# Kernel tuning notes

Measured on AMD Instinct MI355X. Metric: run time of the kernel, lower is better.

The kernel has to match this reference:

```python
import jax, jax.numpy as jnp
import numpy as np

DIM = 2048
N_HEADS = 16
QK_NOPE = 128
QK_ROPE = 64
V_DIM = 128
QK_DIM = QK_NOPE + QK_ROPE  # 192
B, S = 2, 2048


def setup_inputs() -> dict:
    key = jax.random.key(0)
    ks = jax.random.split(key, 6)
    x = jax.random.normal(ks[0], (B, S, DIM), dtype=jnp.float32)
    # rotary angles: theta[j] = 10000^{-2j/d}, angle[p, j] = p * theta[j]
    inv_freq = 1.0 / (10000.0 ** (np.arange(0, QK_ROPE, 2, dtype=np.float32) / QK_ROPE))
    freqs = jnp.asarray(np.arange(S, dtype=np.float32)[:, None] * inv_freq[None, :])  # [S, QK_ROPE//2]
    # additive causal mask
    mask = jnp.where(jnp.tril(jnp.ones((S, S), dtype=bool)), 0.0, -1e9).astype(jnp.float32)
    sc = 1.0 / np.sqrt(DIM)
    wq = jax.random.normal(ks[1], (DIM, N_HEADS * QK_DIM), dtype=jnp.float32) * sc
    wk = jax.random.normal(ks[2], (DIM, N_HEADS * QK_DIM), dtype=jnp.float32) * sc
    wv = jax.random.normal(ks[3], (DIM, N_HEADS * V_DIM), dtype=jnp.float32) * sc
    wo = jax.random.normal(ks[4], (N_HEADS * V_DIM, DIM), dtype=jnp.float32) * (1.0 / np.sqrt(N_HEADS * V_DIM))
    return {"x": x, "start_pos": 0, "freqs": freqs, "mask": mask,
            "wq": wq, "wk": wk, "wv": wv, "wo": wo}


def _apply_rope(t, freqs):
    # t: [B, S, H, D_rope]; freqs: [S, D_rope//2] angles
    b, s, h, d = t.shape
    tr = t.reshape(b, s, h, d // 2, 2)
    cos = jnp.cos(freqs)[None, :, None, :]
    sin = jnp.sin(freqs)[None, :, None, :]
    out = jnp.stack([tr[..., 0] * cos - tr[..., 1] * sin,
                     tr[..., 0] * sin + tr[..., 1] * cos], axis=-1)
    return out.reshape(b, s, h, d)


def reference(x, start_pos, freqs, mask, wq, wk, wv, wo):
    b, s, _ = x.shape
    xq = x @ wq  # [B,S,H*QK_DIM]
    xk = x @ wk
    xv = (x @ wv).reshape(b, s, N_HEADS, V_DIM)
    qnope, qrope = jnp.split(xq, [N_HEADS * QK_NOPE], axis=-1)
    knope, krope = jnp.split(xk, [N_HEADS * QK_NOPE], axis=-1)
    qnope = qnope.reshape(b, s, N_HEADS, QK_NOPE)
    knope = knope.reshape(b, s, N_HEADS, QK_NOPE)
    qrope = _apply_rope(qrope.reshape(b, s, N_HEADS, QK_ROPE), freqs)
    krope = _apply_rope(krope.reshape(b, s, N_HEADS, QK_ROPE), freqs)
    q = jnp.concatenate([qnope, qrope], axis=-1)  # [B,S,H,QK_DIM]
    k = jnp.concatenate([knope, krope], axis=-1)
    scale = 1.0 / jnp.sqrt(jnp.asarray(QK_DIM, dtype=q.dtype))
    scores = jnp.einsum('bqhd,bkhd->bhqk', q, k) * scale
    scores = scores + mask[None, None, :, :]
    attn = jax.nn.softmax(scores.astype(jnp.float32), axis=-1).astype(scores.dtype)
    out = jnp.einsum('bhqk,bkhd->bqhd', attn, xv)  # [B,S,H,V_DIM]
    out = out.reshape(b, s, N_HEADS * V_DIM)
    return out @ wo
```

## Files before the change

### kernel.cpp

```cpp
#include <hip/hip_runtime.h>
#include <hip/hip_bf16.h>

typedef __attribute__((ext_vector_type(4))) float f32x4;
typedef __attribute__((ext_vector_type(8))) short s16x8;
typedef unsigned int u32;
typedef unsigned short u16;

#define GLDS16(gp, lp) __builtin_amdgcn_global_load_lds(                         \
    (const __attribute__((address_space(1))) u32*)(gp),                          \
    (__attribute__((address_space(3))) u32*)(lp), 16, 0, 0)
#define VMCNT4 asm volatile("s_waitcnt vmcnt(4)" ::: "memory")
#define VMCNT0 asm volatile("s_waitcnt vmcnt(0)" ::: "memory")
#define LGKM8  asm volatile("s_waitcnt lgkmcnt(8)" ::: "memory")
#define LGKM0  asm volatile("s_waitcnt lgkmcnt(0)" ::: "memory")
#define SBAR   __builtin_amdgcn_sched_barrier(0)

__device__ __forceinline__ u16 f2bf(float f) {
    u32 u = __builtin_bit_cast(u32, f);
    u32 r = (u + 0x7FFFu + ((u >> 16) & 1u)) >> 16;
    return (u16)r;
}
__device__ __forceinline__ float bf2f(u16 h) {
    u32 u = ((u32)h) << 16;
    return __builtin_bit_cast(float, u);
}

__global__ __launch_bounds__(256) void prep(const float4* __restrict__ x,
                                            ushort4* __restrict__ xb4,
                                            const float* __restrict__ wq,
                                            const float* __restrict__ wk,
                                            const float* __restrict__ wv,
                                            const float* __restrict__ wo,
                                            u16* __restrict__ WT,
                                            u16* __restrict__ woT) {
    __shared__ float tile[32][33];
    int bid = blockIdx.x;
    if (bid < 8192) {
        int i = bid * 256 + threadIdx.x;
        float4 v = x[i];
        ushort4 o;
        o.x = f2bf(v.x); o.y = f2bf(v.y); o.z = f2bf(v.z); o.w = f2bf(v.w);
        xb4[i] = o;
        return;
    }
    bid -= 8192;
    const float* src;
    u16* dst;
    int N, bx, by;
    if (bid < 6144)       { src = wq; dst = WT;                        N = 3072; bx = bid % 96; by = bid / 96; }
    else if (bid < 12288) { bid -= 6144;  src = wk; dst = WT + (size_t)3072 * 2048; N = 3072; bx = bid % 96; by = bid / 96; }
    else if (bid < 16384) { bid -= 12288; src = wv; dst = WT + (size_t)6144 * 2048; N = 2048; bx = bid % 64; by = bid / 64; }
    else                  { bid -= 16384; src = wo; dst = woT;         N = 2048; bx = bid % 64; by = bid / 64; }
    int n0 = bx * 32, k0 = by * 32;
    int tx = threadIdx.x & 31, ty = threadIdx.x >> 5;
#pragma unroll
    for (int i = 0; i < 4; ++i)
        tile[ty + i * 8][tx] = src[(size_t)(k0 + ty + i * 8) * N + n0 + tx];
    __syncthreads();
#pragma unroll
    for (int i = 0; i < 4; ++i) {
        int n = ty + i * 8;
        dst[(size_t)(n0 + n) * 2048 + k0 + tx] = f2bf(tile[tx][n]);
    }
}

__global__ __launch_bounds__(512, 2) void gemm_qkv(const u16* __restrict__ A,
                                                   const u16* __restrict__ W,
                                                   u16* __restrict__ Qh,
                                                   u16* __restrict__ Kh,
                                                   u16* __restrict__ Vn) {
    __shared__ __align__(16) u16 S[2][2][2][128 * 64];
    const int tid = threadIdx.x, lane = tid & 63, wid = tid >> 6;
    const int l15 = lane & 15, l4 = lane >> 4;
    const int id = blockIdx.x;
    const int nt = ((id & 7) << 2) + ((id >> 3) & 3);
    const int mt = id >> 5;
    const int bm0 = mt << 8, bn0 = nt << 8;
    const int wr = wid >> 2, wc = wid & 3;
    f32x4 acc[8][4] = {};

    auto stageH = [&](int mat, int tt, int h) {
        const int kc = tt << 6, p = tt & 1;
        const u16* G = mat ? W : A;
        const int rbase = (mat ? bn0 : bm0) + (h << 7);
        u16* Ld = S[mat][p][h];
#pragma unroll
        for (int j = 0; j < 2; ++j) {
            int c = j * 512 + tid;
            int row = c >> 3, ch = c & 7;
            int cs = ch ^ (row & 7);
            GLDS16(G + (size_t)(rbase + row) * 2048 + kc + cs * 8,
                   (char*)Ld + (j * 512 + wid * 64) * 16);
        }
    };

    s16x8 af[2][2], bfr[4][2];

#define RDA(P, I)                                                              \
    _Pragma("unroll") for (int mm = 0; mm < 2; ++mm)                           \
    _Pragma("unroll") for (int kk = 0; kk < 2; ++kk) {                         \
        int r7 = ((I) * 2 + mm) * 16 + l15;                                    \
        int byt = r7 * 128 + (((kk * 4 + l4) ^ (r7 & 7)) << 4);                \
        af[mm][kk] = *(const s16x8*)((const char*)S[0][P][wr] + byt);          \
    }
#define RDB(P)                                                                 \
    _Pragma("unroll") for (int n = 0; n < 4; ++n)                              \
    _Pragma("unroll") for (int kk = 0; kk < 2; ++kk) {                         \
        int r7 = (wc & 1) * 64 + n * 16 + l15;                                 \
        int byt = r7 * 128 + (((kk * 4 + l4) ^ (r7 & 7)) << 4);                \
        bfr[n][kk] = *(const s16x8*)((const char*)S[1][P][wc >> 1] + byt);     \
    }
#define MF(I)                                                                  \
    __builtin_amdgcn_s_setprio(1);                                             \
    _Pragma("unroll") for (int mm = 0; mm < 2; ++mm)                           \
    _Pragma("unroll") for (int n = 0; n < 4; ++n)                              \
    _Pragma("unroll") for (int kk = 0; kk < 2; ++kk)                           \
        acc[(I) * 2 + mm][n] = __builtin_amdgcn_mfma_f32_16x16x32_bf16(        \
            af[mm][kk], bfr[n][kk], acc[(I) * 2 + mm][n], 0, 0, 0);            \
    __builtin_amdgcn_s_setprio(0);

    stageH(0, 0, 0); stageH(0, 0, 1); stageH(1, 0, 0); stageH(1, 0, 1);
    stageH(0, 1, 0); stageH(0, 1, 1);
    VMCNT4;
    __builtin_amdgcn_s_barrier();
    SBAR;

    for (int t = 0; t < 32; ++t) {
        const int p = t & 1;
        RDB(p); RDA(p, 0);
        if (t == 0) stageH(1, 1, 0);
        else if (t < 31) stageH(0, t + 1, 0);
        LGKM8; SBAR;
        __builtin_amdgcn_s_barrier();
        LGKM0; SBAR;
        MF(0); SBAR;
        __builtin_amdgcn_s_barrier();
        RDA(p, 1);
        if (t == 0) stageH(1, 1, 1);
        else if (t < 31) stageH(0, t + 1, 1);
        __builtin_amdgcn_s_barrier();
        LGKM0; SBAR;
        MF(1); SBAR;
        __builtin_amdgcn_s_barrier();
        RDA(p, 2);
        if (t < 30) stageH(1, t + 2, 0);
        __builtin_amdgcn_s_barrier();
        LGKM0; SBAR;
        MF(2); SBAR;
        __builtin_amdgcn_s_barrier();
        RDA(p, 3);
        if (t < 30) stageH(1, t + 2, 1);
        __builtin_amdgcn_s_barrier();
        LGKM0; SBAR;
        MF(3); SBAR;
        if (t < 31) {
            if (t < 30) { VMCNT4; } else { VMCNT0; }
            SBAR;
        }
        __builtin_amdgcn_s_barrier();
    }
#undef RDA
#undef RDB
#undef MF

#pragma unroll
    for (int m = 0; m < 8; ++m)
#pragma unroll
        for (int n = 0; n < 4; ++n)
#pragma unroll
            for (int r = 0; r < 4; ++r) {
                int row = bm0 + wr * 128 + m * 16 + l4 * 4 + r;
                int c = bn0 + wc * 64 + n * 16 + l15;
                float v = acc[m][n][r];
                if (bn0 >= 6144) {
                    Vn[(size_t)row * 2048 + (c - 6144)] = f2bf(v);
                } else {
                    u16* dst = (bn0 >= 3072) ? Kh : Qh;
                    int cc = (bn0 >= 3072) ? c - 3072 : c;
                    int b = row >> 11, s = row & 2047;
                    int h, d;
                    if (cc < 2048) { h = cc >> 7; d = cc & 127; }
                    else { int mm = cc - 2048; h = mm >> 6; d = 128 + (mm & 63); }
                    dst[(((size_t)b * 16 + h) * 2048 + s) * 192 + d] = f2bf(v);
                }
            }
}

__global__ __launch_bounds__(256) void gemm_bt_f32(const u16* __restrict__ A,
                                                   const u16* __restrict__ Bt,
                                                   float* __restrict__ C,
                                                   int M, int N, int K) {
    __shared__ __align__(16) u16 As[128 * 64];
    __shared__ __align__(16) u16 Bs[128 * 64];
    const int tid = threadIdx.x, lane = tid & 63, wid = tid >> 6;
    const int l15 = lane & 15, l4 = lane >> 4;
    const int bm0 = blockIdx.y << 7, bn0 = blockIdx.x << 7;
    const int wr = wid >> 1, wc = wid & 1;
    f32x4 acc[4][4] = {};
    const int nk = K >> 6;
    for (int t = 0; t < nk; ++t) {
        const int k0 = t << 6;
#pragma unroll
        for (int i = 0; i < 4; ++i) {
            int c = i * 256 + tid;
            int row = c >> 3, c8 = c & 7;
            GLDS16(A + (size_t)(bm0 + row) * K + k0 + c8 * 8,
                   (char*)As + (i * 256 + wid * 64) * 16);
        }
#pragma unroll
        for (int i = 0; i < 4; ++i) {
            int c = i * 256 + tid;
            int row = c >> 3, c8 = c & 7;
            GLDS16(Bt + (size_t)(bn0 + row) * K + k0 + c8 * 8,
                   (char*)Bs + (i * 256 + wid * 64) * 16);
        }
        __syncthreads();
#pragma unroll
        for (int kk = 0; kk < 64; kk += 32) {
            s16x8 af[4], bfr[4];
#pragma unroll
            for (int m = 0; m < 4; ++m)
                af[m] = *(const s16x8*)(As + (wr * 64 + m * 16 + l15) * 64 + kk + l4 * 8);
#pragma unroll
            for (int n = 0; n < 4; ++n)
                bfr[n] = *(const s16x8*)(Bs + (wc * 64 + n * 16 + l15) * 64 + kk + l4 * 8);
#pragma unroll
            for (int m = 0; m < 4; ++m)
#pragma unroll
                for (int n = 0; n < 4; ++n)
                    acc[m][n] = __builtin_amdgcn_mfma_f32_16x16x32_bf16(af[m], bfr[n],
                                                                        acc[m][n], 0, 0, 0);
        }
        __syncthreads();
    }
#pragma unroll
    for (int m = 0; m < 4; ++m)
#pragma unroll
        for (int n = 0; n < 4; ++n)
#pragma unroll
            for (int r = 0; r < 4; ++r) {
                int row = bm0 + wr * 64 + m * 16 + l4 * 4 + r;
                int col = bn0 + wc * 64 + n * 16 + l15;
                C[(size_t)row * N + col] = acc[m][n][r];
            }
}

__global__ __launch_bounds__(256) void rope_inplace(u16* __restrict__ T,
                                                    const float* __restrict__ freqs) {
    int idx = blockIdx.x * 256 + threadIdx.x;
    int j = idx & 31, s = (idx >> 5) & 2047, bh = idx >> 16;
    float ang = freqs[s * 32 + j];
    float c = cosf(ang), sn = sinf(ang);
    u32* p = (u32*)(T + ((size_t)bh * 2048 + s) * 192 + 128) + j;
    u32 v = *p;
    float t0 = bf2f((u16)(v & 0xffff)), t1 = bf2f((u16)(v >> 16));
    float o0 = t0 * c - t1 * sn;
    float o1 = t0 * sn + t1 * c;
    *p = (u32)f2bf(o0) | ((u32)f2bf(o1) << 16);
}

__global__ __launch_bounds__(256) void vtrans(const u16* __restrict__ Vn,
                                              u16* __restrict__ Vt) {
    __shared__ u16 tile[32][33];
    int s0 = blockIdx.x * 32, d0 = blockIdx.y * 32, bh = blockIdx.z;
    int b = bh >> 4, h = bh & 15;
    int tx = threadIdx.x & 31, ty = threadIdx.x >> 5;
#pragma unroll
    for (int i = 0; i < 4; ++i) {
        int s = ty + i * 8;
        tile[s][tx] = Vn[((size_t)b * 2048 + s0 + s) * 2048 + h * 128 + d0 + tx];
    }
    __syncthreads();
#pragma unroll
    for (int i = 0; i < 4; ++i) {
        int d = ty + i * 8;
        Vt[((size_t)bh * 128 + d0 + d) * 2048 + s0 + tx] = tile[tx][d];
    }
}

__global__ __launch_bounds__(256) void attn_fwd3(const u16* __restrict__ Qh,
                                                 const u16* __restrict__ Kh,
                                                 const u16* __restrict__ Vt,
                                                 u16* __restrict__ AO) {
    __shared__ __align__(16) u16 Ks[64 * 192];
    __shared__ __align__(16) u16 Vs[128 * 64];
    __shared__ __align__(16) u16 Ps[4][32 * 64];
    const int tid = threadIdx.x, lane = tid & 63, wid = tid >> 6;
    const int l15 = lane & 15, l4 = lane >> 4;
    const int id = blockIdx.x;
    const int bh = id & 31;
    const int qt = 15 - (id >> 5);
    const int q0 = qt << 7;
    const u16* Qb = Qh + ((size_t)bh * 2048 + q0 + wid * 32) * 192;
    const u16* Kb = Kh + (size_t)bh * 2048 * 192;
    const u16* Vb = Vt + (size_t)bh * 128 * 2048;

    s16x8 aq[2][6];
#pragma unroll
    for (int qg = 0; qg < 2; ++qg)
#pragma unroll
        for (int dk = 0; dk < 6; ++dk)
            aq[qg][dk] = *(const s16x8*)(Qb + (size_t)(qg * 16 + l15) * 192 + dk * 32 + l4 * 8);

    f32x4 acc[2][8] = {};
    float mrow[2][4], lpart[2][4];
#pragma unroll
    for (int qg = 0; qg < 2; ++qg)
#pragma unroll
        for (int r = 0; r < 4; ++r) { mrow[qg][r] = -1e30f; lpart[qg][r] = 0.f; }
    const float scale = 0.07216878364870322f;

    const int ntile = (qt + 1) << 1;
    for (int t = 0; t < ntile; ++t) {
        const int k0 = t << 6;
#pragma unroll
        for (int i = 0; i < 6; ++i) {
            int c = i * 256 + tid;
            int row = (u32)c / 24u, cc = c - row * 24;
            int cs = (cc & 24) | ((cc ^ row) & 7);
            GLDS16(Kb + (size_t)(k0 + row) * 192 + cs * 8,
                   (char*)Ks + (i * 256 + wid * 64) * 16);
        }
#pragma unroll
        for (int i = 0; i < 4; ++i) {
            int c = i * 256 + tid;
            int d = c >> 3, cc = c & 7;
            int cs = cc ^ (d & 7);
            GLDS16(Vb + (size_t)d * 2048 + k0 + cs * 8,
                   (char*)Vs + (i * 256 + wid * 64) * 16);
        }
        __syncthreads();

        if (q0 + wid * 32 + 31 >= k0) {
            f32x4 sc[2][4];
#pragma unroll
            for (int qg = 0; qg < 2; ++qg)
#pragma unroll
                for (int kg = 0; kg < 4; ++kg) sc[qg][kg] = f32x4{0.f, 0.f, 0.f, 0.f};
            __builtin_amdgcn_s_setprio(1);
#pragma unroll
            for (int dk = 0; dk < 6; ++dk) {
                s16x8 bk[4];
#pragma unroll
                for (int kg = 0; kg < 4; ++kg) {
                    int row = kg * 16 + l15;
                    int byt = (row * 384 + dk * 64 + l4 * 16) ^ ((row & 7) << 4);
                    bk[kg] = *(const s16x8*)((const char*)Ks + byt);
                }
#pragma unroll
                for (int qg = 0; qg < 2; ++qg)
#pragma unroll
                    for (int kg = 0; kg < 4; ++kg)
                        sc[qg][kg] = __builtin_amdgcn_mfma_f32_16x16x32_bf16(
                            aq[qg][dk], bk[kg], sc[qg][kg], 0, 0, 0);
            }
            __builtin_amdgcn_s_setprio(0);

            u16* Pw = Ps[wid];
#pragma unroll
            for (int qg = 0; qg < 2; ++qg) {
                const int qrow = q0 + wid * 32 + qg * 16 + l4 * 4;
                const bool domask = (k0 + 63 > qrow);
                float p[4][4], tm[4];
#pragma unroll
                for (int r = 0; r < 4; ++r) tm[r] = -1e30f;
#pragma unroll
                for (int kg = 0; kg < 4; ++kg)
#pragma unroll
                    for (int r = 0; r < 4; ++r) {
                        float v = sc[qg][kg][r] * scale;
                        if (domask && (k0 + kg * 16 + l15 > qrow + r)) v = -1e30f;
                        p[kg][r] = v;
                        tm[r] = fmaxf(tm[r], v);
                    }
#pragma unroll
                for (int off = 1; off < 16; off <<= 1)
#pragma unroll
                    for (int r = 0; r < 4; ++r)
                        tm[r] = fmaxf(tm[r], __shfl_xor(tm[r], off, 64));
                float mn[4];
                bool resc = false;
#pragma unroll
                for (int r = 0; r < 4; ++r) {
                    mn[r] = (tm[r] <= mrow[qg][r] + 8.f) ? mrow[qg][r] : tm[r];
                    resc |= (mn[r] > mrow[qg][r]);
                }
                if (__any(resc)) {
#pragma unroll
                    for (int r = 0; r < 4; ++r) {
                        float scl = __expf(mrow[qg][r] - mn[r]);
                        mrow[qg][r] = mn[r];
                        lpart[qg][r] *= scl;
#pragma unroll
                        for (int db = 0; db < 8; ++db) acc[qg][db][r] *= scl;
                    }
                }
#pragma unroll
                for (int kg = 0; kg < 4; ++kg)
#pragma unroll
                    for (int r = 0; r < 4; ++r) {
                        p[kg][r] = __expf(p[kg][r] - mrow[qg][r]);
                        lpart[qg][r] += p[kg][r];
                    }
#pragma unroll
                for (int kg = 0; kg < 4; ++kg)
#pragma unroll
                    for (int r = 0; r < 4; ++r) {
                        int row = qg * 16 + l4 * 4 + r;
                        int byt = ((row * 64 + kg * 16 + l15) * 2) ^ ((row & 7) << 4);
                        *(u16*)((char*)Pw + byt) = f2bf(p[kg][r]);
                    }
            }

            __builtin_amdgcn_s_setprio(1);
#pragma unroll
            for (int kk = 0; kk < 2; ++kk) {
                s16x8 ap[2];
#pragma unroll
                for (int qg = 0; qg < 2; ++qg) {
                    int row = qg * 16 + l15;
                    int byt = ((row * 64 + kk * 32 + l4 * 8) * 2) ^ ((row & 7) << 4);
                    ap[qg] = *(const s16x8*)((const char*)Pw + byt);
                }
#pragma unroll
                for (int db = 0; db < 8; ++db) {
                    int row = db * 16 + l15;
                    int byt = (row * 128 + kk * 64 + l4 * 16) ^ ((row & 7) << 4);
                    s16x8 bv = *(const s16x8*)((const char*)Vs + byt);
#pragma unroll
                    for (int qg = 0; qg < 2; ++qg)
                        acc[qg][db] = __builtin_amdgcn_mfma_f32_16x16x32_bf16(
                            ap[qg], bv, acc[qg][db], 0, 0, 0);
                }
            }
            __builtin_amdgcn_s_setprio(0);
        }
        __syncthreads();
    }

#pragma unroll
    for (int off = 1; off < 16; off <<= 1)
#pragma unroll
        for (int qg = 0; qg < 2; ++qg)
#pragma unroll
            for (int r = 0; r < 4; ++r)
                lpart[qg][r] += __shfl_xor(lpart[qg][r], off, 64);

    const int b = bh >> 4, h = bh & 15;
#pragma unroll
    for (int qg = 0; qg < 2; ++qg) {
        float inv[4];
#pragma unroll
        for (int r = 0; r < 4; ++r) inv[r] = 1.f / lpart[qg][r];
#pragma unroll
        for (int db = 0; db < 8; ++db)
#pragma unroll
            for (int r = 0; r < 4; ++r) {
                int row = q0 + wid * 32 + qg * 16 + l4 * 4 + r;
                AO[((size_t)b * 2048 + row) * 2048 + h * 128 + db * 16 + l15] =
                    f2bf(acc[qg][db][r] * inv[r]);
            }
    }
}

extern "C" void kernel_launch(void* const* d_in, const int* in_sizes, int n_in,
                              void* d_out, int out_size, void* d_ws, size_t ws_size,
                              hipStream_t stream) {
    const float* x     = (const float*)d_in[0];
    const float* freqs = (const float*)d_in[2];
    const float* wq    = (const float*)d_in[4];
    const float* wk    = (const float*)d_in[5];
    const float* wv    = (const float*)d_in[6];
    const float* wo    = (const float*)d_in[7];
    float* out = (float*)d_out;

    char* ws = (char*)d_ws;
    u16* xb   = (u16*)(ws + 0);
    u16* WT   = (u16*)(ws + 16777216);
    u16* woT  = (u16*)(ws + 50331648);
    u16* Qh   = (u16*)(ws + 58720256);
    u16* Kh   = (u16*)(ws + 83886080);
    u16* Vn   = (u16*)(ws + 109051904);
    u16* Vt   = (u16*)(ws + 125829120);
    u16* AO   = (u16*)(ws + 142606336);

    prep<<<28672, 256, 0, stream>>>((const float4*)x, (ushort4*)xb,
                                    wq, wk, wv, wo, WT, woT);
    gemm_qkv<<<dim3(512), 512, 0, stream>>>(xb, WT, Qh, Kh, Vn);
    rope_inplace<<<8192, 256, 0, stream>>>(Qh, freqs);
    rope_inplace<<<8192, 256, 0, stream>>>(Kh, freqs);
    vtrans<<<dim3(64, 4, 32), 256, 0, stream>>>(Vn, Vt);
    attn_fwd3<<<dim3(512), 256, 0, stream>>>(Qh, Kh, Vt, AO);
    gemm_bt_f32<<<dim3(16, 32), 256, 0, stream>>>(AO, woT, out, 4096, 2048, 2048);
}
```

Measured before the change: 349.7 us.

## Double-buffer K/V tiles in attention and write V transposed from QKV GEMM

```diff
diff --git a/kernel.cpp b/kernel.cpp
--- a/kernel.cpp
+++ b/kernel.cpp
@@ -9,6 +9,7 @@
 #define GLDS16(gp, lp) __builtin_amdgcn_global_load_lds(                         \
     (const __attribute__((address_space(1))) u32*)(gp),                          \
     (__attribute__((address_space(3))) u32*)(lp), 16, 0, 0)
+#define VMCNT10 asm volatile("s_waitcnt vmcnt(10)" ::: "memory")
 #define VMCNT4 asm volatile("s_waitcnt vmcnt(4)" ::: "memory")
 #define VMCNT0 asm volatile("s_waitcnt vmcnt(0)" ::: "memory")
 #define LGKM8  asm volatile("s_waitcnt lgkmcnt(8)" ::: "memory")
@@ -68,7 +69,7 @@
                                                    const u16* __restrict__ W,
                                                    u16* __restrict__ Qh,
                                                    u16* __restrict__ Kh,
-                                                   u16* __restrict__ Vn) {
+                                                   u16* __restrict__ Vt) {
     __shared__ __align__(16) u16 S[2][2][2][128 * 64];
     const int tid = threadIdx.x, lane = tid & 63, wid = tid >> 6;
     const int l15 = lane & 15, l4 = lane >> 4;
@@ -172,12 +173,14 @@
                 int row = bm0 + wr * 128 + m * 16 + l4 * 4 + r;
                 int c = bn0 + wc * 64 + n * 16 + l15;
                 float v = acc[m][n][r];
+                int b = row >> 11, s = row & 2047;
                 if (bn0 >= 6144) {
-                    Vn[(size_t)row * 2048 + (c - 6144)] = f2bf(v);
+                    int cc = c - 6144;
+                    int h = cc >> 7, d = cc & 127;
+                    Vt[(((size_t)(b * 16 + h)) * 128 + d) * 2048 + s] = f2bf(v);
                 } else {
                     u16* dst = (bn0 >= 3072) ? Kh : Qh;
                     int cc = (bn0 >= 3072) ? c - 3072 : c;
-                    int b = row >> 11, s = row & 2047;
                     int h, d;
                     if (cc < 2048) { h = cc >> 7; d = cc & 127; }
                     else { int mm = cc - 2048; h = mm >> 6; d = 128 + (mm & 63); }
@@ -259,31 +262,12 @@
     *p = (u32)f2bf(o0) | ((u32)f2bf(o1) << 16);
 }
 
-__global__ __launch_bounds__(256) void vtrans(const u16* __restrict__ Vn,
-                                              u16* __restrict__ Vt) {
-    __shared__ u16 tile[32][33];
-    int s0 = blockIdx.x * 32, d0 = blockIdx.y * 32, bh = blockIdx.z;
-    int b = bh >> 4, h = bh & 15;
-    int tx = threadIdx.x & 31, ty = threadIdx.x >> 5;
-#pragma unroll
-    for (int i = 0; i < 4; ++i) {
-        int s = ty + i * 8;
-        tile[s][tx] = Vn[((size_t)b * 2048 + s0 + s) * 2048 + h * 128 + d0 + tx];
-    }
-    __syncthreads();
-#pragma unroll
-    for (int i = 0; i < 4; ++i) {
-        int d = ty + i * 8;
-        Vt[((size_t)bh * 128 + d0 + d) * 2048 + s0 + tx] = tile[tx][d];
-    }
-}
-
 __global__ __launch_bounds__(256) void attn_fwd3(const u16* __restrict__ Qh,
                                                  const u16* __restrict__ Kh,
                                                  const u16* __restrict__ Vt,
                                                  u16* __restrict__ AO) {
-    __shared__ __align__(16) u16 Ks[64 * 192];
-    __shared__ __align__(16) u16 Vs[128 * 64];
+    __shared__ __align__(16) u16 Ks[2][64 * 192];
+    __shared__ __align__(16) u16 Vs[2][128 * 64];
     __shared__ __align__(16) u16 Ps[4][32 * 64];
     const int tid = threadIdx.x, lane = tid & 63, wid = tid >> 6;
     const int l15 = lane & 15, l4 = lane >> 4;
@@ -295,23 +279,7 @@
     const u16* Kb = Kh + (size_t)bh * 2048 * 192;
     const u16* Vb = Vt + (size_t)bh * 128 * 2048;
 
-    s16x8 aq[2][6];
-#pragma unroll
-    for (int qg = 0; qg < 2; ++qg)
-#pragma unroll
-        for (int dk = 0; dk < 6; ++dk)
-            aq[qg][dk] = *(const s16x8*)(Qb + (size_t)(qg * 16 + l15) * 192 + dk * 32 + l4 * 8);
-
-    f32x4 acc[2][8] = {};
-    float mrow[2][4], lpart[2][4];
-#pragma unroll
-    for (int qg = 0; qg < 2; ++qg)
-#pragma unroll
-        for (int r = 0; r < 4; ++r) { mrow[qg][r] = -1e30f; lpart[qg][r] = 0.f; }
-    const float scale = 0.07216878364870322f;
-
-    const int ntile = (qt + 1) << 1;
-    for (int t = 0; t < ntile; ++t) {
+    auto stageKV = [&](int t, int buf) {
         const int k0 = t << 6;
 #pragma unroll
         for (int i = 0; i < 6; ++i) {
@@ -319,7 +287,7 @@
             int row = (u32)c / 24u, cc = c - row * 24;
             int cs = (cc & 24) | ((cc ^ row) & 7);
             GLDS16(Kb + (size_t)(k0 + row) * 192 + cs * 8,
-                   (char*)Ks + (i * 256 + wid * 64) * 16);
+                   (char*)Ks[buf] + (i * 256 + wid * 64) * 16);
         }
 #pragma unroll
         for (int i = 0; i < 4; ++i) {
@@ -327,11 +295,43 @@
             int d = c >> 3, cc = c & 7;
             int cs = cc ^ (d & 7);
             GLDS16(Vb + (size_t)d * 2048 + k0 + cs * 8,
-                   (char*)Vs + (i * 256 + wid * 64) * 16);
-        }
-        __syncthreads();
+                   (char*)Vs[buf] + (i * 256 + wid * 64) * 16);
+        }
+    };
+
+    s16x8 aq[2][6];
+#pragma unroll
+    for (int qg = 0; qg < 2; ++qg)
+#pragma unroll
+        for (int dk = 0; dk < 6; ++dk)
+            aq[qg][dk] = *(const s16x8*)(Qb + (size_t)(qg * 16 + l15) * 192 + dk * 32 + l4 * 8);
+
+    f32x4 acc[2][8] = {};
+    float mrow[2][4], lpart[2][4];
+#pragma unroll
+    for (int qg = 0; qg < 2; ++qg)
+#pragma unroll
+        for (int r = 0; r < 4; ++r) { mrow[qg][r] = -1e30f; lpart[qg][r] = 0.f; }
+    const float scale = 0.07216878364870322f;
+
+    const int ntile = (qt + 1) << 1;
+    stageKV(0, 0);
+    for (int t = 0; t < ntile; ++t) {
+        const int cur = t & 1;
+        const int k0 = t << 6;
+        if (t + 1 < ntile) {
+            stageKV(t + 1, cur ^ 1);
+            VMCNT10;
+        } else {
+            VMCNT0;
+        }
+        SBAR;
+        __builtin_amdgcn_s_barrier();
+        SBAR;
 
         if (q0 + wid * 32 + 31 >= k0) {
+            const u16* Kc = Ks[cur];
+            const u16* Vc = Vs[cur];
             f32x4 sc[2][4];
 #pragma unroll
             for (int qg = 0; qg < 2; ++qg)
@@ -345,7 +345,7 @@
                 for (int kg = 0; kg < 4; ++kg) {
                     int row = kg * 16 + l15;
                     int byt = (row * 384 + dk * 64 + l4 * 16) ^ ((row & 7) << 4);
-                    bk[kg] = *(const s16x8*)((const char*)Ks + byt);
+                    bk[kg] = *(const s16x8*)((const char*)Kc + byt);
                 }
 #pragma unroll
                 for (int qg = 0; qg < 2; ++qg)
@@ -426,7 +426,7 @@
                 for (int db = 0; db < 8; ++db) {
                     int row = db * 16 + l15;
                     int byt = (row * 128 + kk * 64 + l4 * 16) ^ ((row & 7) << 4);
-                    s16x8 bv = *(const s16x8*)((const char*)Vs + byt);
+                    s16x8 bv = *(const s16x8*)((const char*)Vc + byt);
 #pragma unroll
                     for (int qg = 0; qg < 2; ++qg)
                         acc[qg][db] = __builtin_amdgcn_mfma_f32_16x16x32_bf16(
@@ -435,7 +435,9 @@
             }
             __builtin_amdgcn_s_setprio(0);
         }
-        __syncthreads();
+        SBAR;
+        __builtin_amdgcn_s_barrier();
+        SBAR;
     }
 
 #pragma unroll
@@ -480,16 +482,14 @@
     u16* woT  = (u16*)(ws + 50331648);
     u16* Qh   = (u16*)(ws + 58720256);
     u16* Kh   = (u16*)(ws + 83886080);
-    u16* Vn   = (u16*)(ws + 109051904);
     u16* Vt   = (u16*)(ws + 125829120);
     u16* AO   = (u16*)(ws + 142606336);
 
     prep<<<28672, 256, 0, stream>>>((const float4*)x, (ushort4*)xb,
                                     wq, wk, wv, wo, WT, woT);
-    gemm_qkv<<<dim3(512), 512, 0, stream>>>(xb, WT, Qh, Kh, Vn);
+    gemm_qkv<<<dim3(512), 512, 0, stream>>>(xb, WT, Qh, Kh, Vt);
     rope_inplace<<<8192, 256, 0, stream>>>(Qh, freqs);
     rope_inplace<<<8192, 256, 0, stream>>>(Kh, freqs);
-    vtrans<<<dim3(64, 4, 32), 256, 0, stream>>>(Vn, Vt);
     attn_fwd3<<<dim3(512), 256, 0, stream>>>(Qh, Kh, Vt, AO);
     gemm_bt_f32<<<dim3(16, 32), 256, 0, stream>>>(AO, woT, out, 4096, 2048, 2048);
 }
```

Result: slower. 380.6 us (+8.8%).

## Double-buffer K tiles and overlap next-tile K and V loads with compute

Applied to the files above, without the earlier changes.

```diff
diff --git a/kernel.cpp b/kernel.cpp
--- a/kernel.cpp
+++ b/kernel.cpp
@@ -9,6 +9,8 @@
 #define GLDS16(gp, lp) __builtin_amdgcn_global_load_lds(                         \
     (const __attribute__((address_space(1))) u32*)(gp),                          \
     (__attribute__((address_space(3))) u32*)(lp), 16, 0, 0)
+#define VMCNT10 asm volatile("s_waitcnt vmcnt(10)" ::: "memory")
+#define VMCNT6 asm volatile("s_waitcnt vmcnt(6)" ::: "memory")
 #define VMCNT4 asm volatile("s_waitcnt vmcnt(4)" ::: "memory")
 #define VMCNT0 asm volatile("s_waitcnt vmcnt(0)" ::: "memory")
 #define LGKM8  asm volatile("s_waitcnt lgkmcnt(8)" ::: "memory")
@@ -282,7 +284,7 @@
                                                  const u16* __restrict__ Kh,
                                                  const u16* __restrict__ Vt,
                                                  u16* __restrict__ AO) {
-    __shared__ __align__(16) u16 Ks[64 * 192];
+    __shared__ __align__(16) u16 Ks[2][64 * 192];
     __shared__ __align__(16) u16 Vs[128 * 64];
     __shared__ __align__(16) u16 Ps[4][32 * 64];
     const int tid = threadIdx.x, lane = tid & 63, wid = tid >> 6;
@@ -295,23 +297,7 @@
     const u16* Kb = Kh + (size_t)bh * 2048 * 192;
     const u16* Vb = Vt + (size_t)bh * 128 * 2048;
 
-    s16x8 aq[2][6];
-#pragma unroll
-    for (int qg = 0; qg < 2; ++qg)
-#pragma unroll
-        for (int dk = 0; dk < 6; ++dk)
-            aq[qg][dk] = *(const s16x8*)(Qb + (size_t)(qg * 16 + l15) * 192 + dk * 32 + l4 * 8);
-
-    f32x4 acc[2][8] = {};
-    float mrow[2][4], lpart[2][4];
-#pragma unroll
-    for (int qg = 0; qg < 2; ++qg)
-#pragma unroll
-        for (int r = 0; r < 4; ++r) { mrow[qg][r] = -1e30f; lpart[qg][r] = 0.f; }
-    const float scale = 0.07216878364870322f;
-
-    const int ntile = (qt + 1) << 1;
-    for (int t = 0; t < ntile; ++t) {
+    auto stageK = [&](int t, int buf) {
         const int k0 = t << 6;
 #pragma unroll
         for (int i = 0; i < 6; ++i) {
@@ -319,8 +305,11 @@
             int row = (u32)c / 24u, cc = c - row * 24;
             int cs = (cc & 24) | ((cc ^ row) & 7);
             GLDS16(Kb + (size_t)(k0 + row) * 192 + cs * 8,
-                   (char*)Ks + (i * 256 + wid * 64) * 16);
-        }
+                   (char*)Ks[buf] + (i * 256 + wid * 64) * 16);
+        }
+    };
+    auto stageV = [&](int t) {
+        const int k0 = t << 6;
 #pragma unroll
         for (int i = 0; i < 4; ++i) {
             int c = i * 256 + tid;
@@ -329,9 +318,39 @@
             GLDS16(Vb + (size_t)d * 2048 + k0 + cs * 8,
                    (char*)Vs + (i * 256 + wid * 64) * 16);
         }
-        __syncthreads();
-
-        if (q0 + wid * 32 + 31 >= k0) {
+    };
+
+    s16x8 aq[2][6];
+#pragma unroll
+    for (int qg = 0; qg < 2; ++qg)
+#pragma unroll
+        for (int dk = 0; dk < 6; ++dk)
+            aq[qg][dk] = *(const s16x8*)(Qb + (size_t)(qg * 16 + l15) * 192 + dk * 32 + l4 * 8);
+
+    f32x4 acc[2][8] = {};
+    float mrow[2][4], lpart[2][4];
+#pragma unroll
+    for (int qg = 0; qg < 2; ++qg)
+#pragma unroll
+        for (int r = 0; r < 4; ++r) { mrow[qg][r] = -1e30f; lpart[qg][r] = 0.f; }
+    const float scale = 0.07216878364870322f;
+
+    const int ntile = (qt + 1) << 1;
+    stageK(0, 0);
+    for (int t = 0; t < ntile; ++t) {
+        const int cur = t & 1;
+        const int k0 = t << 6;
+        const bool pf = (t + 1 < ntile);
+        stageV(t);
+        if (pf) stageK(t + 1, cur ^ 1);
+        if (pf) { VMCNT10; } else { VMCNT4; }
+        SBAR;
+        __builtin_amdgcn_s_barrier();
+        SBAR;
+
+        const bool live = (q0 + wid * 32 + 31 >= k0);
+        if (live) {
+            const u16* Kc = Ks[cur];
             f32x4 sc[2][4];
 #pragma unroll
             for (int qg = 0; qg < 2; ++qg)
@@ -345,7 +364,7 @@
                 for (int kg = 0; kg < 4; ++kg) {
                     int row = kg * 16 + l15;
                     int byt = (row * 384 + dk * 64 + l4 * 16) ^ ((row & 7) << 4);
-                    bk[kg] = *(const s16x8*)((const char*)Ks + byt);
+                    bk[kg] = *(const s16x8*)((const char*)Kc + byt);
                 }
 #pragma unroll
                 for (int qg = 0; qg < 2; ++qg)
@@ -411,7 +430,15 @@
                         *(u16*)((char*)Pw + byt) = f2bf(p[kg][r]);
                     }
             }
-
+        }
+
+        if (pf) { VMCNT6; } else { VMCNT0; }
+        SBAR;
+        __builtin_amdgcn_s_barrier();
+        SBAR;
+
+        if (live) {
+            u16* Pw = Ps[wid];
             __builtin_amdgcn_s_setprio(1);
 #pragma unroll
             for (int kk = 0; kk < 2; ++kk) {
@@ -435,7 +462,9 @@
             }
             __builtin_amdgcn_s_setprio(0);
         }
-        __syncthreads();
+        SBAR;
+        __builtin_amdgcn_s_barrier();
+        SBAR;
     }
 
 #pragma unroll
```

New measurement: 349.2 us. Within noise of the previous version (-0.2%).
